# Kernel tuning notes

Hardware: AMD Instinct MI355X
Metric: run time of the kernel (lower is better)

Reference implementation:

```python
import jax, jax.numpy as jnp
import numpy as np

SPACE = 63
STRIDE = 2
TEMP = 0.07
W_CHAR, W_WORD, W_PHRASE, W_IDEA = 1.0, 0.5, 0.1, 0.1


def setup_inputs() -> dict:
    key = jax.random.key(0)
    ks = jax.random.split(key, 6)
    B, S, V, D = 8, 4096, 256, 512
    return {
        "logits": jax.random.normal(ks[0], (B, S, V), jnp.float32),
        "word_preds": jax.random.normal(ks[1], (B, D, S // STRIDE), jnp.float32),
        "char_features": jax.random.normal(ks[2], (B, D, S), jnp.float32),
        "contrastive_2": jax.random.normal(ks[3], (B, 128, 1024), jnp.float32),
        "contrastive_3": jax.random.normal(ks[4], (B, 128, 256), jnp.float32),
        "targets": jax.random.randint(ks[5], (B, S), 0, V, jnp.int32),
        "mask": jnp.ones((B, S), jnp.float32),
    }


def _info_nce(emb, temp=TEMP):
    # emb: (B, dim, L). Anchors = even positions, positives = odd positions.
    B, dim, L = emb.shape
    n_pairs = L // 2
    a = emb[:, :, 0:2 * n_pairs:2].transpose(0, 2, 1).reshape(-1, dim)
    p = emb[:, :, 1:2 * n_pairs:2].transpose(0, 2, 1).reshape(-1, dim)
    a = a / jnp.maximum(jnp.linalg.norm(a, axis=1, keepdims=True), 1e-12)
    p = p / jnp.maximum(jnp.linalg.norm(p, axis=1, keepdims=True), 1e-12)
    logits = (a @ p.T) / temp  # (n, n)
    n = logits.shape[0]
    logp = jax.nn.log_softmax(logits, axis=1)
    idx = jnp.arange(n)
    return -jnp.mean(logp[idx, idx])


def _word_span_loss(word_preds, char_features, targets, stride=STRIDE):
    # Segment-mean over spans between consecutive spaces; MSE vs gathered preds.
    B, D, S = char_features.shape
    Wlen = word_preds.shape[2]
    nseg = S + 2  # segment k in [1, n_spaces-1] = span after the k-th space; last slot = junk
    space = targets == SPACE
    cs = jnp.cumsum(space.astype(jnp.int32), axis=1)  # inclusive space count
    seg = jnp.where(space, nseg - 1, cs)          # non-space chars -> span id
    seg_sp = jnp.where(space, cs, nseg - 1)       # space positions -> their space index k
    t_idx = jnp.arange(S, dtype=jnp.int32)

    def per_batch(feats, seg_b, seg_sp_b):
        sums = jax.ops.segment_sum(feats.T, seg_b, num_segments=nseg)  # (nseg, D)
        cnts = jax.ops.segment_sum(jnp.ones((S,), feats.dtype), seg_b, num_segments=nseg)
        pos = jnp.full((nseg,), S, jnp.int32).at[seg_sp_b].set(t_idx)  # position of k-th space
        return sums, cnts, pos

    sums, cnts, pos = jax.vmap(per_batch)(char_features, seg, seg_sp)
    n_sp = cs[:, -1]  # (B,)
    k = jnp.arange(nseg)[None, :]
    valid = (k >= 1) & (k <= n_sp[:, None] - 1) & (cnts > 0) & ((pos // stride) < Wlen)
    means = jax.lax.stop_gradient(sums / jnp.maximum(cnts, 1.0)[..., None])  # target.detach()
    wp = jnp.clip(pos // stride, 0, Wlen - 1)  # (B, nseg)
    preds = jnp.take_along_axis(word_preds.transpose(0, 2, 1), wp[:, :, None], axis=1)  # (B,nseg,D)
    mse = jnp.mean((preds - means) ** 2, axis=-1)  # per-span F.mse_loss (mean over feat dim)
    tot = jnp.sum(jnp.where(valid, mse, 0.0))
    cnt = jnp.sum(valid).astype(mse.dtype)
    return jnp.where(cnt > 0, tot / jnp.maximum(cnt, 1.0), 0.0)


def reference(logits, word_preds, char_features, contrastive_2, contrastive_3, targets, mask):
    # char CE with mask
    logp = jax.nn.log_softmax(logits, axis=-1)
    ce = -jnp.take_along_axis(logp, targets[..., None].astype(jnp.int32), axis=-1)[..., 0]
    n = jnp.sum(mask)
    char_loss = jnp.where(n > 0, jnp.sum(ce * mask) / jnp.maximum(n, 1.0), jnp.mean(ce))
    word_loss = _word_span_loss(word_preds, char_features, targets)
    phrase_loss = _info_nce(contrastive_2)
    idea_loss = _info_nce(contrastive_3)
    return (W_CHAR * char_loss + W_WORD * word_loss
            + W_PHRASE * phrase_loss + W_IDEA * idea_loss)
```

## Files before the change

kernel.cpp:

```cpp
#include <hip/hip_runtime.h>

#define SPACE_TOK 63
#define INV_T 14.285714285714286f
#define SA_SCALE 20.609929155556595f
#define LN2F 0.6931471805599453f

typedef __attribute__((ext_vector_type(8))) short bf16x8;
typedef __attribute__((ext_vector_type(4))) float f32x4;

#define O_NSP    0
#define O_SPPOS  64
#define O_CECM   131136
#define O_CEM    135232
#define O_CEC    139328
#define O_WPART  143424
#define O_WCNT   159808
#define O_PEXP2  160832
#define O_PEXP3  291904
#define O_DIAG2  324672
#define O_DIAG3  341056
#define O_A2     345152
#define SZ_A2    (4096*128*2)
#define O_P2     (O_A2 + SZ_A2)
#define O_A3     (O_P2 + SZ_A2)
#define SZ_A3    (1024*128*2)
#define O_P3     (O_A3 + SZ_A3)

#define SMEM_A 18048

__device__ inline unsigned short f2bf(float x) {
  union { float f; unsigned int u; } c; c.f = x;
  unsigned int r = c.u + 0x7fffu + ((c.u >> 16) & 1u);
  return (unsigned short)(r >> 16);
}

__device__ void scan_body(char* smem, const int* __restrict__ targets, char* ws, int b) {
  int tid = threadIdx.x;
  int* toks = (int*)smem;
  int* sc   = (int*)(smem + 16384);
  int* n_sp   = (int*)(ws + O_NSP);
  int* sp_pos = (int*)(ws + O_SPPOS);
  const int4* tb4 = (const int4*)(targets + b * 4096);
#pragma unroll
  for (int i = 0; i < 4; ++i) ((int4*)toks)[tid + 256 * i] = tb4[tid + 256 * i];
  __syncthreads();
  int base = tid * 16;
  int cnt = 0;
#pragma unroll
  for (int i = 0; i < 16; ++i) cnt += (toks[base + i] == SPACE_TOK);
  sc[tid] = cnt;
  __syncthreads();
  for (int off = 1; off < 256; off <<= 1) {
    int v = (tid >= off) ? sc[tid - off] : 0;
    __syncthreads();
    sc[tid] += v;
    __syncthreads();
  }
  int k = sc[tid] - cnt;
  for (int i = 0; i < 16; ++i)
    if (toks[base + i] == SPACE_TOK) sp_pos[b * 4096 + (k++)] = base + i;
  if (tid == 255) n_sp[b] = sc[255];
}

__device__ void norm_body(char* smem, const float* __restrict__ emb, int L,
                          unsigned short* __restrict__ Abf, unsigned short* __restrict__ Pbf,
                          int b, int l0) {
  float (*tile)[33] = (float(*)[33])smem;
  float (*np8)[32]  = (float(*)[32])(smem + 16896);
  float* scl        = (float*)(smem + 16896 + 1024);
  int tid = threadIdx.x;
  int lx = tid & 31, cq = tid >> 5;
  const float* eb = emb + (size_t)b * 128 * L + l0;
  for (int c = cq; c < 128; c += 8) tile[c][lx] = eb[(size_t)c * L + lx];
  __syncthreads();
  {
    float s = 0.f;
    for (int c = cq; c < 128; c += 8) { float x = tile[c][lx]; s += x * x; }
    np8[cq][lx] = s;
  }
  __syncthreads();
  if (tid < 32) {
    float t = 0.f;
#pragma unroll
    for (int g = 0; g < 8; ++g) t += np8[g][tid];
    float nrm = fmaxf(sqrtf(t), 1e-12f);
    scl[tid] = ((tid & 1) ? 1.0f : SA_SCALE) / nrm;
  }
  __syncthreads();
  int c = tid & 127, lh = tid >> 7;
  int half = L >> 1;
  for (int lp = lh; lp < 32; lp += 2) {
    int l = l0 + lp;
    int row = b * half + (l >> 1);
    unsigned short v = f2bf(tile[c][lp] * scl[lp]);
    ((l & 1) ? Pbf : Abf)[(size_t)row * 128 + c] = v;
  }
}

__device__ void ce_body(char* smem, const float* __restrict__ logits,
                        const int* __restrict__ targets, const float* __restrict__ mask,
                        char* ws, int cb) {
  int tid = threadIdx.x;
  int wave = tid >> 6, lane = tid & 63;
  int rbase = cb * 32 + wave * 8;
  float4 v[8];
  float mk[8];
  int tg[8];
#pragma unroll
  for (int rr = 0; rr < 8; ++rr) v[rr] = ((const float4*)logits)[(size_t)(rbase + rr) * 64 + lane];
#pragma unroll
  for (int rr = 0; rr < 8; ++rr) { tg[rr] = targets[rbase + rr]; mk[rr] = mask[rbase + rr]; }
  float aCM = 0.f, aM = 0.f, aC = 0.f;
#pragma unroll
  for (int rr = 0; rr < 8; ++rr) {
    float e = __expf(v[rr].x) + __expf(v[rr].y) + __expf(v[rr].z) + __expf(v[rr].w);
#pragma unroll
    for (int m = 1; m < 64; m <<= 1) e += __shfl_xor(e, m);
    int t = tg[rr];
    int q = t & 3;
    float sel = (q == 0) ? v[rr].x : (q == 1) ? v[rr].y : (q == 2) ? v[rr].z : v[rr].w;
    float xt = __shfl(sel, t >> 2);
    float ce = __logf(e) - xt;
    aCM += ce * mk[rr]; aM += mk[rr]; aC += ce;
  }
  float (*red)[3] = (float(*)[3])smem;
  if (lane == 0) { red[wave][0] = aCM; red[wave][1] = aM; red[wave][2] = aC; }
  __syncthreads();
  if (tid == 0) {
    ((float*)(ws + O_CECM))[cb] = red[0][0] + red[1][0] + red[2][0] + red[3][0];
    ((float*)(ws + O_CEM ))[cb] = red[0][1] + red[1][1] + red[2][1] + red[3][1];
    ((float*)(ws + O_CEC ))[cb] = red[0][2] + red[1][2] + red[2][2] + red[3][2];
  }
}

__global__ void __launch_bounds__(256) fusedA_kernel(const float* __restrict__ logits,
                                                     const int* __restrict__ targets,
                                                     const float* __restrict__ mask,
                                                     const float* __restrict__ c2,
                                                     const float* __restrict__ c3,
                                                     char* __restrict__ ws) {
  extern __shared__ char smem[];
  int bid = blockIdx.x;
  if (bid < 8) {
    scan_body(smem, targets, ws, bid);
  } else if (bid < 264) {
    int nb = bid - 8;
    norm_body(smem, c2, 1024, (unsigned short*)(ws + O_A2), (unsigned short*)(ws + O_P2),
              nb & 7, (nb >> 3) * 32);
  } else if (bid < 328) {
    int nb = bid - 264;
    norm_body(smem, c3, 256, (unsigned short*)(ws + O_A3), (unsigned short*)(ws + O_P3),
              nb & 7, (nb >> 3) * 32);
  } else {
    ce_body(smem, logits, targets, mask, ws, bid - 328);
  }
}

__device__ void nce_body(char* smem, const unsigned short* __restrict__ A,
                         const unsigned short* __restrict__ P, int n, int sliceJ,
                         int blk_i, int s, float* __restrict__ pexp,
                         float* __restrict__ diag) {
  int tid = threadIdx.x;
  int wave = tid >> 6, lane = tid & 63;
  int col = lane & 15, quad = lane >> 4;
  int I0 = blk_i * 16;
  const unsigned short* Ap = A + (size_t)(I0 + col) * 128 + quad * 8;
  bf16x8 a0 = *(const bf16x8*)(Ap);
  bf16x8 a1 = *(const bf16x8*)(Ap + 32);
  bf16x8 a2 = *(const bf16x8*)(Ap + 64);
  bf16x8 a3 = *(const bf16x8*)(Ap + 96);
  float rl0 = 0.f, rl1 = 0.f, rl2 = 0.f, rl3 = 0.f;
  float dcap = 0.f;
  int perW = sliceJ >> 2;
  int J0w = s * sliceJ + wave * perW, Jend = J0w + perW;
#pragma unroll 2
  for (int J = J0w; J < Jend; J += 16) {
    const unsigned short* Pp = P + (size_t)(J + col) * 128 + quad * 8;
    bf16x8 b0 = *(const bf16x8*)(Pp);
    bf16x8 b1 = *(const bf16x8*)(Pp + 32);
    bf16x8 b2 = *(const bf16x8*)(Pp + 64);
    bf16x8 b3 = *(const bf16x8*)(Pp + 96);
    f32x4 cfr = {0.f, 0.f, 0.f, 0.f};
    cfr = __builtin_amdgcn_mfma_f32_16x16x32_bf16(a0, b0, cfr, 0, 0, 0);
    cfr = __builtin_amdgcn_mfma_f32_16x16x32_bf16(a1, b1, cfr, 0, 0, 0);
    cfr = __builtin_amdgcn_mfma_f32_16x16x32_bf16(a2, b2, cfr, 0, 0, 0);
    cfr = __builtin_amdgcn_mfma_f32_16x16x32_bf16(a3, b3, cfr, 0, 0, 0);
    rl0 += exp2f(cfr[0] - SA_SCALE);
    rl1 += exp2f(cfr[1] - SA_SCALE);
    rl2 += exp2f(cfr[2] - SA_SCALE);
    rl3 += exp2f(cfr[3] - SA_SCALE);
    if (J == I0) {
      int r = col - (quad << 2);
      if (r == 0) dcap = cfr[0];
      else if (r == 1) dcap = cfr[1];
      else if (r == 2) dcap = cfr[2];
      else if (r == 3) dcap = cfr[3];
    }
  }
  float (*part)[16][16] = (float(*)[16][16])smem;
  float (*dpart)[16]    = (float(*)[16])(smem + 4096);
  part[wave][(quad << 2) + 0][col] = rl0;
  part[wave][(quad << 2) + 1][col] = rl1;
  part[wave][(quad << 2) + 2][col] = rl2;
  part[wave][(quad << 2) + 3][col] = rl3;
  if (quad == (col >> 2)) dpart[wave][col] = dcap;
  __syncthreads();
  {
    int rrow = tid >> 4, cc = tid & 15;
    float sv = 0.f, d = 0.f;
#pragma unroll
    for (int w = 0; w < 4; ++w) { sv += part[w][rrow][cc]; d += dpart[w][rrow]; }
#pragma unroll
    for (int m = 1; m < 16; m <<= 1) sv += __shfl_xor(sv, m);
    if (cc == 0) {
      pexp[I0 + rrow] = sv;
      if (I0 >= s * sliceJ && I0 < (s + 1) * sliceJ) diag[I0 + rrow] = d;
    }
  }
}

__device__ void word_body(char* smem, const float* __restrict__ wp,
                          const float* __restrict__ cf, char* ws, int w) {
  int b = w & 7, y = (w >> 3) & 31, z = w >> 8;
  int ns = ((const int*)(ws + O_NSP))[b];
  const int* sp_pos = (const int*)(ws + O_SPPOS);
  int wave = threadIdx.x >> 6, lane = threadIdx.x & 63;
  int dbase = z * 32 + wave * 8;
  float myacc = 0.f;
  float lcnt = 0.f;
  for (int k = 1 + y; k <= ns - 1; k += 32) {
    int t0 = sp_pos[b * 4096 + k - 1];
    int t1 = sp_pos[b * 4096 + k];
    int cnt = t1 - t0 - 1;
    if (cnt <= 0) continue;
    lcnt += 1.0f;
    int wpos = t0 >> 1;
    float invc = 1.0f / (float)cnt;
    const float* r0 = cf + ((size_t)(b * 512 + dbase)) * 4096;
    int c0 = (t0 + 1) >> 2;
    int c1 = (t1 + 3) >> 2;
    float s0 = 0.f, s1 = 0.f, s2 = 0.f, s3 = 0.f, s4 = 0.f, s5 = 0.f, s6 = 0.f, s7 = 0.f;
    for (int c = c0 + lane; c < c1; c += 64) {
      int tb = c << 2;
      float4 v0 = *(const float4*)(r0 + 0 * 4096 + tb);
      float4 v1 = *(const float4*)(r0 + 1 * 4096 + tb);
      float4 v2 = *(const float4*)(r0 + 2 * 4096 + tb);
      float4 v3 = *(const float4*)(r0 + 3 * 4096 + tb);
      float4 v4 = *(const float4*)(r0 + 4 * 4096 + tb);
      float4 v5 = *(const float4*)(r0 + 5 * 4096 + tb);
      float4 v6 = *(const float4*)(r0 + 6 * 4096 + tb);
      float4 v7 = *(const float4*)(r0 + 7 * 4096 + tb);
      float m0 = (tb + 0 > t0 && tb + 0 < t1) ? 1.f : 0.f;
      float m1 = (tb + 1 > t0 && tb + 1 < t1) ? 1.f : 0.f;
      float m2 = (tb + 2 > t0 && tb + 2 < t1) ? 1.f : 0.f;
      float m3 = (tb + 3 > t0 && tb + 3 < t1) ? 1.f : 0.f;
      s0 += v0.x * m0 + v0.y * m1 + v0.z * m2 + v0.w * m3;
      s1 += v1.x * m0 + v1.y * m1 + v1.z * m2 + v1.w * m3;
      s2 += v2.x * m0 + v2.y * m1 + v2.z * m2 + v2.w * m3;
      s3 += v3.x * m0 + v3.y * m1 + v3.z * m2 + v3.w * m3;
      s4 += v4.x * m0 + v4.y * m1 + v4.z * m2 + v4.w * m3;
      s5 += v5.x * m0 + v5.y * m1 + v5.z * m2 + v5.w * m3;
      s6 += v6.x * m0 + v6.y * m1 + v6.z * m2 + v6.w * m3;
      s7 += v7.x * m0 + v7.y * m1 + v7.z * m2 + v7.w * m3;
    }
#pragma unroll
    for (int m = 1; m < 64; m <<= 1) {
      s0 += __shfl_xor(s0, m); s1 += __shfl_xor(s1, m);
      s2 += __shfl_xor(s2, m); s3 += __shfl_xor(s3, m);
      s4 += __shfl_xor(s4, m); s5 += __shfl_xor(s5, m);
      s6 += __shfl_xor(s6, m); s7 += __shfl_xor(s7, m);
    }
    if (lane < 8) {
      float sv = (lane == 0) ? s0 : (lane == 1) ? s1 : (lane == 2) ? s2 : (lane == 3) ? s3
               : (lane == 4) ? s4 : (lane == 5) ? s5 : (lane == 6) ? s6 : s7;
      float mean = sv * invc;
      float pred = wp[((size_t)(b * 512 + dbase + lane)) * 2048 + wpos];
      float diff = pred - mean;
      myacc += diff * diff;
    }
  }
#pragma unroll
  for (int m = 1; m < 8; m <<= 1) myacc += __shfl_xor(myacc, m);
  float* wacc = (float*)smem;
  if (lane == 0) wacc[wave] = myacc;
  __syncthreads();
  if (threadIdx.x == 0) {
    ((float*)(ws + O_WPART))[w] = (wacc[0] + wacc[1] + wacc[2] + wacc[3]) * (1.0f / 512.0f);
    if (z == 0) ((float*)(ws + O_WCNT))[w] = lcnt;
  }
}

__global__ void __launch_bounds__(256) fusedB_kernel(const float* __restrict__ wp,
                                                     const float* __restrict__ cf,
                                                     char* __restrict__ ws) {
  extern __shared__ char smem[];
  int bid = blockIdx.x;
  if (bid < 2048) {
    nce_body(smem, (const unsigned short*)(ws + O_A2), (const unsigned short*)(ws + O_P2),
             4096, 512, bid >> 3, bid & 7,
             (float*)(ws + O_PEXP2) + (bid & 7) * 4096, (float*)(ws + O_DIAG2));
  } else if (bid < 2560) {
    int nb = bid - 2048;
    nce_body(smem, (const unsigned short*)(ws + O_A3), (const unsigned short*)(ws + O_P3),
             1024, 128, nb >> 3, nb & 7,
             (float*)(ws + O_PEXP3) + (nb & 7) * 1024, (float*)(ws + O_DIAG3));
  } else {
    word_body(smem, wp, cf, ws, bid - 2560);
  }
}

__global__ void __launch_bounds__(256) final_kernel(const char* __restrict__ ws,
                                                    float* __restrict__ out) {
  int tid = threadIdx.x;
  int wave = tid >> 6, lane = tid & 63;
  const float* cecm  = (const float*)(ws + O_CECM);
  const float* cem   = (const float*)(ws + O_CEM);
  const float* cec   = (const float*)(ws + O_CEC);
  const float* wpart = (const float*)(ws + O_WPART);
  const float* wcnt  = (const float*)(ws + O_WCNT);
  const float* p2    = (const float*)(ws + O_PEXP2);
  const float* p3    = (const float*)(ws + O_PEXP3);
  const float* dg2   = (const float*)(ws + O_DIAG2);
  const float* dg3   = (const float*)(ws + O_DIAG3);
  float v[7] = {0.f, 0.f, 0.f, 0.f, 0.f, 0.f, 0.f};
  for (int i = tid; i < 1024; i += 256) { v[0] += cecm[i]; v[1] += cem[i]; v[2] += cec[i]; }
  for (int i = tid; i < 4096; i += 256) v[3] += wpart[i];
  v[4] = wcnt[tid];
  for (int r = tid; r < 4096; r += 256) {
    float S = 0.f;
#pragma unroll
    for (int s = 0; s < 8; ++s) S += p2[s * 4096 + r];
    v[5] += INV_T + __logf(S) - LN2F * dg2[r];
  }
  for (int r = tid; r < 1024; r += 256) {
    float S = 0.f;
#pragma unroll
    for (int s = 0; s < 8; ++s) S += p3[s * 1024 + r];
    v[6] += INV_T + __logf(S) - LN2F * dg3[r];
  }
#pragma unroll
  for (int j = 0; j < 7; ++j) {
    float x = v[j];
#pragma unroll
    for (int m = 1; m < 64; m <<= 1) x += __shfl_xor(x, m);
    v[j] = x;
  }
  __shared__ float fr[4][7];
  if (lane == 0)
#pragma unroll
    for (int j = 0; j < 7; ++j) fr[wave][j] = v[j];
  __syncthreads();
  if (tid == 0) {
    float s[7];
#pragma unroll
    for (int j = 0; j < 7; ++j) s[j] = fr[0][j] + fr[1][j] + fr[2][j] + fr[3][j];
    float n = s[1];
    float charL = (n > 0.f) ? (s[0] / fmaxf(n, 1.f)) : (s[2] / 32768.0f);
    float wordL = (s[4] > 0.f) ? (s[3] / fmaxf(s[4], 1.f)) : 0.f;
    out[0] = charL + 0.5f * wordL + 0.1f * (s[5] / 4096.0f) + 0.1f * (s[6] / 1024.0f);
  }
}

extern "C" void kernel_launch(void* const* d_in, const int* in_sizes, int n_in,
                              void* d_out, int out_size, void* d_ws, size_t ws_size,
                              hipStream_t stream) {
  (void)in_sizes; (void)n_in; (void)out_size; (void)ws_size;
  const float* logits        = (const float*)d_in[0];
  const float* word_preds    = (const float*)d_in[1];
  const float* char_features = (const float*)d_in[2];
  const float* c2            = (const float*)d_in[3];
  const float* c3            = (const float*)d_in[4];
  const int*   targets       = (const int*)d_in[5];
  const float* mask          = (const float*)d_in[6];
  float* out = (float*)d_out;
  char* ws = (char*)d_ws;

  fusedA_kernel<<<1352, 256, SMEM_A, stream>>>(logits, targets, mask, c2, c3, ws);
  fusedB_kernel<<<6656, 256, 4480, stream>>>(word_preds, char_features, ws);
  final_kernel<<<1, 256, 0, stream>>>(ws, out);
}
```

Before: 215.9 us.

## Move space scan into standalone word kernel with per-chunk local segment discovery

The global space-position scan in the first fused kernel is removed. A new word kernel scans its own quarter of the targets in shared memory, finds the next space after its chunk, and computes span means and MSE for the spans that start inside it. Word work is split into 512 blocks by batch, token quarter and feature slice, and the contrastive blocks move to a separate kernel. This removes the dependency on a serial scan block and the strided span distribution across blocks. In exchange it adds a fourth launch, redundant token scanning per feature slice, and uneven load when spans are long or cross chunks.

```diff
diff --git a/kernel.cpp b/kernel.cpp
--- a/kernel.cpp
+++ b/kernel.cpp
@@ -8,18 +8,16 @@
 typedef __attribute__((ext_vector_type(8))) short bf16x8;
 typedef __attribute__((ext_vector_type(4))) float f32x4;
 
-#define O_NSP    0
-#define O_SPPOS  64
-#define O_CECM   131136
-#define O_CEM    135232
-#define O_CEC    139328
-#define O_WPART  143424
-#define O_WCNT   159808
-#define O_PEXP2  160832
-#define O_PEXP3  291904
-#define O_DIAG2  324672
-#define O_DIAG3  341056
-#define O_A2     345152
+#define O_CECM   0
+#define O_CEM    4096
+#define O_CEC    8192
+#define O_WPART  12288
+#define O_WCNT   14336
+#define O_PEXP2  14464
+#define O_DIAG2  145536
+#define O_PEXP3  161920
+#define O_DIAG3  194688
+#define O_A2     198784
 #define SZ_A2    (4096*128*2)
 #define O_P2     (O_A2 + SZ_A2)
 #define O_A3     (O_P2 + SZ_A2)
@@ -32,34 +30,6 @@
   union { float f; unsigned int u; } c; c.f = x;
   unsigned int r = c.u + 0x7fffu + ((c.u >> 16) & 1u);
   return (unsigned short)(r >> 16);
-}
-
-__device__ void scan_body(char* smem, const int* __restrict__ targets, char* ws, int b) {
-  int tid = threadIdx.x;
-  int* toks = (int*)smem;
-  int* sc   = (int*)(smem + 16384);
-  int* n_sp   = (int*)(ws + O_NSP);
-  int* sp_pos = (int*)(ws + O_SPPOS);
-  const int4* tb4 = (const int4*)(targets + b * 4096);
-#pragma unroll
-  for (int i = 0; i < 4; ++i) ((int4*)toks)[tid + 256 * i] = tb4[tid + 256 * i];
-  __syncthreads();
-  int base = tid * 16;
-  int cnt = 0;
-#pragma unroll
-  for (int i = 0; i < 16; ++i) cnt += (toks[base + i] == SPACE_TOK);
-  sc[tid] = cnt;
-  __syncthreads();
-  for (int off = 1; off < 256; off <<= 1) {
-    int v = (tid >= off) ? sc[tid - off] : 0;
-    __syncthreads();
-    sc[tid] += v;
-    __syncthreads();
-  }
-  int k = sc[tid] - cnt;
-  for (int i = 0; i < 16; ++i)
-    if (toks[base + i] == SPACE_TOK) sp_pos[b * 4096 + (k++)] = base + i;
-  if (tid == 255) n_sp[b] = sc[255];
 }
 
 __device__ void norm_body(char* smem, const float* __restrict__ emb, int L,
@@ -141,18 +111,136 @@
                                                      char* __restrict__ ws) {
   extern __shared__ char smem[];
   int bid = blockIdx.x;
-  if (bid < 8) {
-    scan_body(smem, targets, ws, bid);
-  } else if (bid < 264) {
-    int nb = bid - 8;
+  if (bid < 256) {
     norm_body(smem, c2, 1024, (unsigned short*)(ws + O_A2), (unsigned short*)(ws + O_P2),
-              nb & 7, (nb >> 3) * 32);
-  } else if (bid < 328) {
-    int nb = bid - 264;
+              bid & 7, (bid >> 3) * 32);
+  } else if (bid < 320) {
+    int nb = bid - 256;
     norm_body(smem, c3, 256, (unsigned short*)(ws + O_A3), (unsigned short*)(ws + O_P3),
               nb & 7, (nb >> 3) * 32);
   } else {
-    ce_body(smem, logits, targets, mask, ws, bid - 328);
+    ce_body(smem, logits, targets, mask, ws, bid - 320);
+  }
+}
+
+__global__ void __launch_bounds__(256) word_kernel(const float* __restrict__ wp,
+                                                   const float* __restrict__ cf,
+                                                   const int* __restrict__ targets,
+                                                   char* __restrict__ ws) {
+  __shared__ int sc[256];
+  __shared__ int splist[1024];
+  __shared__ int snext_sh;
+  __shared__ float wacc[4];
+  int tid = threadIdx.x;
+  int w = blockIdx.x;
+  int z = w & 15, tq = (w >> 4) & 3, b = w >> 6;
+  const int* tb = targets + b * 4096;
+  int tbase = tq * 1024;
+  int4 tok = ((const int4*)(tb + tbase))[tid];
+  int f0 = (tok.x == SPACE_TOK), f1 = (tok.y == SPACE_TOK),
+      f2 = (tok.z == SPACE_TOK), f3 = (tok.w == SPACE_TOK);
+  int cnt = f0 + f1 + f2 + f3;
+  sc[tid] = cnt;
+  __syncthreads();
+  for (int off = 1; off < 256; off <<= 1) {
+    int v = (tid >= off) ? sc[tid - off] : 0;
+    __syncthreads();
+    sc[tid] += v;
+    __syncthreads();
+  }
+  int base = sc[tid] - cnt;
+  int p = tbase + tid * 4;
+  if (f0) splist[base++] = p;
+  if (f1) splist[base++] = p + 1;
+  if (f2) splist[base++] = p + 2;
+  if (f3) splist[base++] = p + 3;
+  int m = sc[255];
+  if (tid == 0) snext_sh = -1;
+  __syncthreads();
+  if (m > 0) {
+    for (int wstart = tbase + 1024; wstart < 4096 && snext_sh < 0; wstart += 1024) {
+      int t = wstart + tid * 4;
+      int4 tk = ((const int4*)tb)[t >> 2];
+      int found = 0x7fffffff;
+      if (tk.x == SPACE_TOK) found = t;
+      else if (tk.y == SPACE_TOK) found = t + 1;
+      else if (tk.z == SPACE_TOK) found = t + 2;
+      else if (tk.w == SPACE_TOK) found = t + 3;
+#pragma unroll
+      for (int mm = 1; mm < 64; mm <<= 1) found = min(found, __shfl_xor(found, mm));
+      if ((tid & 63) == 0) sc[tid >> 6] = found;
+      __syncthreads();
+      if (tid == 0) {
+        int f = min(min(sc[0], sc[1]), min(sc[2], sc[3]));
+        if (f != 0x7fffffff) snext_sh = f;
+      }
+      __syncthreads();
+    }
+  }
+  int snext = snext_sh;
+  int wave = tid >> 6, lane = tid & 63;
+  int dbase = z * 32 + wave * 8;
+  const float* r0 = cf + ((size_t)(b * 512 + dbase)) * 4096;
+  float myacc = 0.f;
+  float lcnt = 0.f;
+  for (int i = 0; i < m; ++i) {
+    int t0 = splist[i];
+    int t1 = (i + 1 < m) ? splist[i + 1] : snext;
+    if (t1 < 0) break;
+    int seglen = t1 - t0 - 1;
+    if (seglen <= 0) continue;
+    lcnt += 1.0f;
+    int wpos = t0 >> 1;
+    float invc = 1.0f / (float)seglen;
+    int c0 = (t0 + 1) >> 2;
+    int c1 = (t1 + 3) >> 2;
+    float s0 = 0.f, s1 = 0.f, s2 = 0.f, s3 = 0.f, s4 = 0.f, s5 = 0.f, s6 = 0.f, s7 = 0.f;
+    for (int c = c0 + lane; c < c1; c += 64) {
+      int tbp = c << 2;
+      float4 v0 = *(const float4*)(r0 + 0 * 4096 + tbp);
+      float4 v1 = *(const float4*)(r0 + 1 * 4096 + tbp);
+      float4 v2 = *(const float4*)(r0 + 2 * 4096 + tbp);
+      float4 v3 = *(const float4*)(r0 + 3 * 4096 + tbp);
+      float4 v4 = *(const float4*)(r0 + 4 * 4096 + tbp);
+      float4 v5 = *(const float4*)(r0 + 5 * 4096 + tbp);
+      float4 v6 = *(const float4*)(r0 + 6 * 4096 + tbp);
+      float4 v7 = *(const float4*)(r0 + 7 * 4096 + tbp);
+      float m0 = (tbp + 0 > t0 && tbp + 0 < t1) ? 1.f : 0.f;
+      float m1 = (tbp + 1 > t0 && tbp + 1 < t1) ? 1.f : 0.f;
+      float m2 = (tbp + 2 > t0 && tbp + 2 < t1) ? 1.f : 0.f;
+      float m3 = (tbp + 3 > t0 && tbp + 3 < t1) ? 1.f : 0.f;
+      s0 += v0.x * m0 + v0.y * m1 + v0.z * m2 + v0.w * m3;
+      s1 += v1.x * m0 + v1.y * m1 + v1.z * m2 + v1.w * m3;
+      s2 += v2.x * m0 + v2.y * m1 + v2.z * m2 + v2.w * m3;
+      s3 += v3.x * m0 + v3.y * m1 + v3.z * m2 + v3.w * m3;
+      s4 += v4.x * m0 + v4.y * m1 + v4.z * m2 + v4.w * m3;
+      s5 += v5.x * m0 + v5.y * m1 + v5.z * m2 + v5.w * m3;
+      s6 += v6.x * m0 + v6.y * m1 + v6.z * m2 + v6.w * m3;
+      s7 += v7.x * m0 + v7.y * m1 + v7.z * m2 + v7.w * m3;
+    }
+#pragma unroll
+    for (int mm = 1; mm < 64; mm <<= 1) {
+      s0 += __shfl_xor(s0, mm); s1 += __shfl_xor(s1, mm);
+      s2 += __shfl_xor(s2, mm); s3 += __shfl_xor(s3, mm);
+      s4 += __shfl_xor(s4, mm); s5 += __shfl_xor(s5, mm);
+      s6 += __shfl_xor(s6, mm); s7 += __shfl_xor(s7, mm);
+    }
+    if (lane < 8) {
+      float sv = (lane == 0) ? s0 : (lane == 1) ? s1 : (lane == 2) ? s2 : (lane == 3) ? s3
+               : (lane == 4) ? s4 : (lane == 5) ? s5 : (lane == 6) ? s6 : s7;
+      float mean = sv * invc;
+      float pred = wp[((size_t)(b * 512 + dbase + lane)) * 2048 + wpos];
+      float diff = pred - mean;
+      myacc += diff * diff;
+    }
+  }
+#pragma unroll
+  for (int mm = 1; mm < 8; mm <<= 1) myacc += __shfl_xor(myacc, mm);
+  if (lane == 0) wacc[wave] = myacc;
+  __syncthreads();
+  if (tid == 0) {
+    ((float*)(ws + O_WPART))[w] = (wacc[0] + wacc[1] + wacc[2] + wacc[3]) * (1.0f / 512.0f);
+    if (z == 0) ((float*)(ws + O_WCNT))[w >> 4] = lcnt;
   }
 }
 
@@ -209,9 +297,9 @@
     int rrow = tid >> 4, cc = tid & 15;
     float sv = 0.f, d = 0.f;
 #pragma unroll
-    for (int w = 0; w < 4; ++w) { sv += part[w][rrow][cc]; d += dpart[w][rrow]; }
-#pragma unroll
-    for (int m = 1; m < 16; m <<= 1) sv += __shfl_xor(sv, m);
+    for (int ww = 0; ww < 4; ++ww) { sv += part[ww][rrow][cc]; d += dpart[ww][rrow]; }
+#pragma unroll
+    for (int mm = 1; mm < 16; mm <<= 1) sv += __shfl_xor(sv, mm);
     if (cc == 0) {
       pexp[I0 + rrow] = sv;
       if (I0 >= s * sliceJ && I0 < (s + 1) * sliceJ) diag[I0 + rrow] = d;
@@ -219,93 +307,18 @@
   }
 }
 
-__device__ void word_body(char* smem, const float* __restrict__ wp,
-                          const float* __restrict__ cf, char* ws, int w) {
-  int b = w & 7, y = (w >> 3) & 31, z = w >> 8;
-  int ns = ((const int*)(ws + O_NSP))[b];
-  const int* sp_pos = (const int*)(ws + O_SPPOS);
-  int wave = threadIdx.x >> 6, lane = threadIdx.x & 63;
-  int dbase = z * 32 + wave * 8;
-  float myacc = 0.f;
-  float lcnt = 0.f;
-  for (int k = 1 + y; k <= ns - 1; k += 32) {
-    int t0 = sp_pos[b * 4096 + k - 1];
-    int t1 = sp_pos[b * 4096 + k];
-    int cnt = t1 - t0 - 1;
-    if (cnt <= 0) continue;
-    lcnt += 1.0f;
-    int wpos = t0 >> 1;
-    float invc = 1.0f / (float)cnt;
-    const float* r0 = cf + ((size_t)(b * 512 + dbase)) * 4096;
-    int c0 = (t0 + 1) >> 2;
-    int c1 = (t1 + 3) >> 2;
-    float s0 = 0.f, s1 = 0.f, s2 = 0.f, s3 = 0.f, s4 = 0.f, s5 = 0.f, s6 = 0.f, s7 = 0.f;
-    for (int c = c0 + lane; c < c1; c += 64) {
-      int tb = c << 2;
-      float4 v0 = *(const float4*)(r0 + 0 * 4096 + tb);
-      float4 v1 = *(const float4*)(r0 + 1 * 4096 + tb);
-      float4 v2 = *(const float4*)(r0 + 2 * 4096 + tb);
-      float4 v3 = *(const float4*)(r0 + 3 * 4096 + tb);
-      float4 v4 = *(const float4*)(r0 + 4 * 4096 + tb);
-      float4 v5 = *(const float4*)(r0 + 5 * 4096 + tb);
-      float4 v6 = *(const float4*)(r0 + 6 * 4096 + tb);
-      float4 v7 = *(const float4*)(r0 + 7 * 4096 + tb);
-      float m0 = (tb + 0 > t0 && tb + 0 < t1) ? 1.f : 0.f;
-      float m1 = (tb + 1 > t0 && tb + 1 < t1) ? 1.f : 0.f;
-      float m2 = (tb + 2 > t0 && tb + 2 < t1) ? 1.f : 0.f;
-      float m3 = (tb + 3 > t0 && tb + 3 < t1) ? 1.f : 0.f;
-      s0 += v0.x * m0 + v0.y * m1 + v0.z * m2 + v0.w * m3;
-      s1 += v1.x * m0 + v1.y * m1 + v1.z * m2 + v1.w * m3;
-      s2 += v2.x * m0 + v2.y * m1 + v2.z * m2 + v2.w * m3;
-      s3 += v3.x * m0 + v3.y * m1 + v3.z * m2 + v3.w * m3;
-      s4 += v4.x * m0 + v4.y * m1 + v4.z * m2 + v4.w * m3;
-      s5 += v5.x * m0 + v5.y * m1 + v5.z * m2 + v5.w * m3;
-      s6 += v6.x * m0 + v6.y * m1 + v6.z * m2 + v6.w * m3;
-      s7 += v7.x * m0 + v7.y * m1 + v7.z * m2 + v7.w * m3;
-    }
-#pragma unroll
-    for (int m = 1; m < 64; m <<= 1) {
-      s0 += __shfl_xor(s0, m); s1 += __shfl_xor(s1, m);
-      s2 += __shfl_xor(s2, m); s3 += __shfl_xor(s3, m);
-      s4 += __shfl_xor(s4, m); s5 += __shfl_xor(s5, m);
-      s6 += __shfl_xor(s6, m); s7 += __shfl_xor(s7, m);
-    }
-    if (lane < 8) {
-      float sv = (lane == 0) ? s0 : (lane == 1) ? s1 : (lane == 2) ? s2 : (lane == 3) ? s3
-               : (lane == 4) ? s4 : (lane == 5) ? s5 : (lane == 6) ? s6 : s7;
-      float mean = sv * invc;
-      float pred = wp[((size_t)(b * 512 + dbase + lane)) * 2048 + wpos];
-      float diff = pred - mean;
-      myacc += diff * diff;
-    }
-  }
-#pragma unroll
-  for (int m = 1; m < 8; m <<= 1) myacc += __shfl_xor(myacc, m);
-  float* wacc = (float*)smem;
-  if (lane == 0) wacc[wave] = myacc;
-  __syncthreads();
-  if (threadIdx.x == 0) {
-    ((float*)(ws + O_WPART))[w] = (wacc[0] + wacc[1] + wacc[2] + wacc[3]) * (1.0f / 512.0f);
-    if (z == 0) ((float*)(ws + O_WCNT))[w] = lcnt;
-  }
-}
-
-__global__ void __launch_bounds__(256) fusedB_kernel(const float* __restrict__ wp,
-                                                     const float* __restrict__ cf,
-                                                     char* __restrict__ ws) {
+__global__ void __launch_bounds__(256) fusedC_kernel(char* __restrict__ ws) {
   extern __shared__ char smem[];
   int bid = blockIdx.x;
   if (bid < 2048) {
     nce_body(smem, (const unsigned short*)(ws + O_A2), (const unsigned short*)(ws + O_P2),
              4096, 512, bid >> 3, bid & 7,
              (float*)(ws + O_PEXP2) + (bid & 7) * 4096, (float*)(ws + O_DIAG2));
-  } else if (bid < 2560) {
+  } else {
     int nb = bid - 2048;
     nce_body(smem, (const unsigned short*)(ws + O_A3), (const unsigned short*)(ws + O_P3),
              1024, 128, nb >> 3, nb & 7,
              (float*)(ws + O_PEXP3) + (nb & 7) * 1024, (float*)(ws + O_DIAG3));
-  } else {
-    word_body(smem, wp, cf, ws, bid - 2560);
   }
 }
 
@@ -313,36 +326,48 @@
                                                     float* __restrict__ out) {
   int tid = threadIdx.x;
   int wave = tid >> 6, lane = tid & 63;
-  const float* cecm  = (const float*)(ws + O_CECM);
-  const float* cem   = (const float*)(ws + O_CEM);
-  const float* cec   = (const float*)(ws + O_CEC);
-  const float* wpart = (const float*)(ws + O_WPART);
-  const float* wcnt  = (const float*)(ws + O_WCNT);
-  const float* p2    = (const float*)(ws + O_PEXP2);
-  const float* p3    = (const float*)(ws + O_PEXP3);
-  const float* dg2   = (const float*)(ws + O_DIAG2);
-  const float* dg3   = (const float*)(ws + O_DIAG3);
   float v[7] = {0.f, 0.f, 0.f, 0.f, 0.f, 0.f, 0.f};
-  for (int i = tid; i < 1024; i += 256) { v[0] += cecm[i]; v[1] += cem[i]; v[2] += cec[i]; }
-  for (int i = tid; i < 4096; i += 256) v[3] += wpart[i];
-  v[4] = wcnt[tid];
-  for (int r = tid; r < 4096; r += 256) {
-    float S = 0.f;
-#pragma unroll
-    for (int s = 0; s < 8; ++s) S += p2[s * 4096 + r];
-    v[5] += INV_T + __logf(S) - LN2F * dg2[r];
-  }
-  for (int r = tid; r < 1024; r += 256) {
-    float S = 0.f;
-#pragma unroll
-    for (int s = 0; s < 8; ++s) S += p3[s * 1024 + r];
-    v[6] += INV_T + __logf(S) - LN2F * dg3[r];
+  {
+    float4 a = ((const float4*)(ws + O_CECM))[tid];
+    float4 bb = ((const float4*)(ws + O_CEM))[tid];
+    float4 c = ((const float4*)(ws + O_CEC))[tid];
+    v[0] = a.x + a.y + a.z + a.w;
+    v[1] = bb.x + bb.y + bb.z + bb.w;
+    v[2] = c.x + c.y + c.z + c.w;
+  }
+  if (tid < 128) {
+    float4 wv = ((const float4*)(ws + O_WPART))[tid];
+    v[3] = wv.x + wv.y + wv.z + wv.w;
+  }
+  if (tid < 32) v[4] = ((const float*)(ws + O_WCNT))[tid];
+  for (int r4 = tid; r4 < 1024; r4 += 256) {
+    float4 S = {0.f, 0.f, 0.f, 0.f};
+#pragma unroll
+    for (int s = 0; s < 8; ++s) {
+      float4 pv = ((const float4*)(ws + O_PEXP2))[s * 1024 + r4];
+      S.x += pv.x; S.y += pv.y; S.z += pv.z; S.w += pv.w;
+    }
+    float4 dg = ((const float4*)(ws + O_DIAG2))[r4];
+    v[5] += 4.0f * INV_T + __logf(S.x) + __logf(S.y) + __logf(S.z) + __logf(S.w)
+            - LN2F * (dg.x + dg.y + dg.z + dg.w);
+  }
+  if (tid < 256) {
+    int r4 = tid;
+    float4 S = {0.f, 0.f, 0.f, 0.f};
+#pragma unroll
+    for (int s = 0; s < 8; ++s) {
+      float4 pv = ((const float4*)(ws + O_PEXP3))[s * 256 + r4];
+      S.x += pv.x; S.y += pv.y; S.z += pv.z; S.w += pv.w;
+    }
+    float4 dg = ((const float4*)(ws + O_DIAG3))[r4];
+    v[6] = 4.0f * INV_T + __logf(S.x) + __logf(S.y) + __logf(S.z) + __logf(S.w)
+           - LN2F * (dg.x + dg.y + dg.z + dg.w);
   }
 #pragma unroll
   for (int j = 0; j < 7; ++j) {
     float x = v[j];
 #pragma unroll
-    for (int m = 1; m < 64; m <<= 1) x += __shfl_xor(x, m);
+    for (int mm = 1; mm < 64; mm <<= 1) x += __shfl_xor(x, mm);
     v[j] = x;
   }
   __shared__ float fr[4][7];
@@ -375,7 +400,8 @@
   float* out = (float*)d_out;
   char* ws = (char*)d_ws;
 
-  fusedA_kernel<<<1352, 256, SMEM_A, stream>>>(logits, targets, mask, c2, c3, ws);
-  fusedB_kernel<<<6656, 256, 4480, stream>>>(word_preds, char_features, ws);
+  fusedA_kernel<<<1344, 256, SMEM_A, stream>>>(logits, targets, mask, c2, c3, ws);
+  word_kernel<<<512, 256, 0, stream>>>(word_preds, char_features, targets, ws);
+  fusedC_kernel<<<2560, 256, 4480, stream>>>(ws);
   final_kernel<<<1, 256, 0, stream>>>(ws, out);
 }
```

After: 212.5 us. Within noise of the previous version (-1.6%).
